# Optimization experiments

Measured on AMD Instinct MI355X. Metric: run time of the kernel, lower is better.

## Reference

```python
import jax, jax.numpy as jnp
import numpy as np

NQ, NT, D = 8192, 8192, 128
EC, EQ, ET = 262144, 262144, 262144


def seg_softmax(logits, seg, num):
    # numerically stable segment softmax over a 1-D logits vector
    m = jax.ops.segment_max(logits, seg, num_segments=num)
    e = jnp.exp(logits - m[seg])
    s = jax.ops.segment_sum(e, seg, num_segments=num)
    return e / s[seg]


def _linear_params(key, din, dout):
    k1, k2 = jax.random.split(key)
    scale = 1.0 / np.sqrt(din)
    W = jax.random.uniform(k1, (din, dout), minval=-scale, maxval=scale, dtype=jnp.float32)
    b = jax.random.uniform(k2, (dout,), minval=-scale, maxval=scale, dtype=jnp.float32)
    return W, b


def setup_inputs():
    key = jax.random.key(0)
    ks = jax.random.split(key, 20)
    inp = {
        'Xq': jax.random.normal(ks[0], (NQ, D), dtype=jnp.float32),
        'edge_index_q': jax.random.randint(ks[1], (2, EQ), 0, NQ),
        'Xt': jax.random.normal(ks[2], (NT, D), dtype=jnp.float32),
        'edge_index_t': jax.random.randint(ks[3], (2, ET), 0, NT),
        'norm_q': jax.random.uniform(ks[4], (NQ, 1), dtype=jnp.float32),
        'norm_t': jax.random.uniform(ks[5], (NT, 1), dtype=jnp.float32),
        'cross_src': jax.random.randint(ks[6], (EC,), 0, NQ),
        'cross_dst': jax.random.randint(ks[7], (EC,), 0, NT),
        'node_mask': jnp.ones((NQ,), dtype=bool),
        'only_run_inter': 0,
    }
    names_dims = [
        ('ac_q', D, D), ('ac_t', D, D), ('vc_q', D, D), ('vc_t', D, D),
        ('mq', 2 * D, D), ('mt', 3 * D, D),
        ('aq', 2 * D, 1), ('vq', 2 * D, D), ('at', 2 * D, 1), ('vt', 2 * D, D),
    ]
    for i, (nm, din, dout) in enumerate(names_dims):
        W, b = _linear_params(ks[8 + i], din, dout)
        inp['W_' + nm] = W
        inp['b_' + nm] = b
    return inp


def reference(Xq, edge_index_q, Xt, edge_index_t, norm_q, norm_t, cross_src, cross_dst,
              node_mask, only_run_inter,
              W_ac_q, b_ac_q, W_ac_t, b_ac_t, W_vc_q, b_vc_q, W_vc_t, b_vc_t,
              W_mq, b_mq, W_mt, b_mt,
              W_aq, b_aq, W_vq, b_vq, W_at, b_at, W_vt, b_vt):
    elu = jax.nn.elu
    nq, nt, d = Xq.shape[0], Xt.shape[0], Xq.shape[1]

    # cross-graph attention logits: per (u, v) pair, dot of transformed features
    Xq_ac = elu(Xq @ W_ac_q + b_ac_q)
    Xt_ac = elu(Xt @ W_ac_t + b_ac_t)
    att_logits = jnp.sum(Xq_ac[cross_src] * Xt_ac[cross_dst], axis=-1)  # [EC]

    # t2q: aggregate target values into query nodes (faithful to original: values gathered by u indices)
    Xt_vc = elu(Xt @ W_vc_t + b_vc_t)
    att_u = seg_softmax(att_logits, cross_src, nq)[:, None]
    Xt2q = jax.ops.segment_sum(att_u * Xt_vc[cross_src], cross_src, num_segments=nq)
    Xq_merged = jnp.concatenate([Xq, Xt2q], axis=1) @ W_mq + b_mq

    # q2t: aggregate query values into target nodes, plus global query summary Q
    Xq_vc = elu(Xq @ W_vc_q + b_vc_q)
    att_v = seg_softmax(att_logits, cross_dst, nt)[:, None]
    Xq2t = jax.ops.segment_sum(att_v * Xq_vc[cross_src], cross_dst, num_segments=nt)
    Q = jnp.broadcast_to(jnp.mean(Xq, axis=0, keepdims=True), (nt, d))
    Xt_merged = jnp.concatenate([Xt, Xq2t, Q], axis=1) @ W_mt + b_mt

    if only_run_inter:
        return Xq_merged, Xt_merged

    # intra-graph edge-wise gather -> MLP -> softmax-scatter message passing
    msg_t = jnp.concatenate([Xt_merged[edge_index_t[0]], Xt_merged[edge_index_t[1]]], axis=1)  # [ET, 2D]
    a_t = seg_softmax((msg_t @ W_at + b_at)[:, 0], edge_index_t[1], nt)[:, None]
    Xt_out = jax.ops.segment_sum(a_t * (msg_t @ W_vt + b_vt), edge_index_t[1], num_segments=nt)

    msg_q = jnp.concatenate([Xq_merged[edge_index_q[0]], Xq_merged[edge_index_q[1]]], axis=1)  # [EQ, 2D]
    a_q = seg_softmax((msg_q @ W_aq + b_aq)[:, 0], edge_index_q[1], nq)[:, None]
    Xq_out = jax.ops.segment_sum(a_q * (msg_q @ W_vq + b_vq), edge_index_q[1], num_segments=nq)

    return Xq_out, Xt_out
```

## Files before the change

kernel.cpp:

```cpp
#include <hip/hip_runtime.h>
#include <math.h>


#define NBIN 8192
#define NB   128
#define DEGCAP 256

typedef _Float16 h2f __attribute__((ext_vector_type(2)));

__device__ __forceinline__ float elu1(float x) { return x > 0.f ? x : __expf(x) - 1.f; }

__device__ __forceinline__ unsigned short f2bf(float x) {
    unsigned u = __float_as_uint(x);
    u += 0x7FFF + ((u >> 16) & 1);
    return (unsigned short)(u >> 16);
}
__device__ __forceinline__ float bflo(unsigned u) { return __uint_as_float(u << 16); }
__device__ __forceinline__ float bfhi(unsigned u) { return __uint_as_float(u & 0xFFFF0000u); }
__device__ __forceinline__ unsigned short f2h(float x) {
    return __builtin_bit_cast(unsigned short, (_Float16)x);
}

__device__ __forceinline__ float dot8_f16(const uint4 a, const uint4 b, float d) {
#if __has_builtin(__builtin_amdgcn_fdot2)
    d = __builtin_amdgcn_fdot2(__builtin_bit_cast(h2f, a.x), __builtin_bit_cast(h2f, b.x), d, false);
    d = __builtin_amdgcn_fdot2(__builtin_bit_cast(h2f, a.y), __builtin_bit_cast(h2f, b.y), d, false);
    d = __builtin_amdgcn_fdot2(__builtin_bit_cast(h2f, a.z), __builtin_bit_cast(h2f, b.z), d, false);
    d = __builtin_amdgcn_fdot2(__builtin_bit_cast(h2f, a.w), __builtin_bit_cast(h2f, b.w), d, false);
#else
    const unsigned ua[4] = { a.x, a.y, a.z, a.w };
    const unsigned ub[4] = { b.x, b.y, b.z, b.w };
    #pragma unroll
    for (int t = 0; t < 4; ++t) {
        const h2f ha = __builtin_bit_cast(h2f, ua[t]);
        const h2f hb = __builtin_bit_cast(h2f, ub[t]);
        d = fmaf((float)ha.x, (float)hb.x, d);
        d = fmaf((float)ha.y, (float)hb.y, d);
    }
#endif
    return d;
}

struct GemmJob {
    const float* A0; const float* A1; const int* rowmask1;
    const float* W00; const float* W01;
    const float* W10; const float* W11;
    const float* bias0; const float* bias1;
    float* C0; float* C1;
    unsigned short* Cb0; unsigned short* Cb1;
    unsigned short* Ch0; unsigned short* Ch1;
    const float* gvw; float* gvo;
    int act;
};

__global__ __launch_bounds__(256) void gemm_big(GemmJob j0, GemmJob j1)
{
    const GemmJob j = blockIdx.z ? j1 : j0;
    const int out = blockIdx.y >> 1;
    const int c0 = (blockIdx.y & 1) * 64;
    const int r0 = blockIdx.x * 128;
    __shared__ float As[32][132];
    __shared__ float Ws[32][64];
    const int tid = threadIdx.x;
    const int tr = tid >> 4, tc = tid & 15;
    float acc[8][4] = {};

    const float* A_pass[2] = { j.A0, j.A1 };
    const float* W_pass[2] = { out ? j.W01 : j.W00, out ? j.W11 : j.W10 };

    for (int p = 0; p < 2; ++p) {
        const float* A = A_pass[p];
        if (!A) break;
        const float* W = W_pass[p];
        const int* rm = (p == 1) ? j.rowmask1 : nullptr;
        for (int kc = 0; kc < 4; ++kc) {
            {
                const int k4 = (tid & 7) * 4;
                const int rb = tid >> 3;
                #pragma unroll
                for (int i = 0; i < 4; ++i) {
                    const int r = rb + 32 * i;
                    float4 v = *(const float4*)(A + (size_t)(r0 + r) * 128 + kc * 32 + k4);
                    if (rm && rm[r0 + r] == 0) v = make_float4(0.f, 0.f, 0.f, 0.f);
                    As[k4 + 0][r] = v.x; As[k4 + 1][r] = v.y;
                    As[k4 + 2][r] = v.z; As[k4 + 3][r] = v.w;
                }
                const int cc = (tid & 15) * 4;
                const int kb = tid >> 4;
                #pragma unroll
                for (int i = 0; i < 2; ++i) {
                    const int k = kb + 16 * i;
                    *(float4*)&Ws[k][cc] = *(const float4*)(W + (size_t)(kc * 32 + k) * 128 + c0 + cc);
                }
            }
            __syncthreads();
            #pragma unroll 4
            for (int k = 0; k < 32; ++k) {
                const float4 a0 = *(const float4*)&As[k][tr * 4];
                const float4 a1 = *(const float4*)&As[k][64 + tr * 4];
                const float4 w  = *(const float4*)&Ws[k][tc * 4];
                const float ar[8] = {a0.x, a0.y, a0.z, a0.w, a1.x, a1.y, a1.z, a1.w};
                #pragma unroll
                for (int i = 0; i < 8; ++i) {
                    acc[i][0] = fmaf(ar[i], w.x, acc[i][0]);
                    acc[i][1] = fmaf(ar[i], w.y, acc[i][1]);
                    acc[i][2] = fmaf(ar[i], w.z, acc[i][2]);
                    acc[i][3] = fmaf(ar[i], w.w, acc[i][3]);
                }
            }
            __syncthreads();
        }
    }

    float4 bv = make_float4(0.f, 0.f, 0.f, 0.f);
    const float* bias = out ? j.bias1 : j.bias0;
    if (bias) bv = *(const float4*)(bias + c0 + tc * 4);
    float* C = out ? j.C1 : j.C0;
    unsigned short* Cb = out ? j.Cb1 : j.Cb0;
    unsigned short* Ch = out ? j.Ch1 : j.Ch0;
    const int dogv = (j.gvw != nullptr) && (out == 0);
    float4 wv4 = make_float4(0.f, 0.f, 0.f, 0.f);
    if (dogv) wv4 = *(const float4*)(j.gvw + c0 + tc * 4);
    float pacc[8];
    #pragma unroll
    for (int i = 0; i < 8; ++i) {
        const int row = r0 + (i >> 2) * 64 + tr * 4 + (i & 3);
        float4 o;
        o.x = acc[i][0] + bv.x; o.y = acc[i][1] + bv.y;
        o.z = acc[i][2] + bv.z; o.w = acc[i][3] + bv.w;
        if (j.act) { o.x = elu1(o.x); o.y = elu1(o.y); o.z = elu1(o.z); o.w = elu1(o.w); }
        pacc[i] = o.x * wv4.x + o.y * wv4.y + o.z * wv4.z + o.w * wv4.w;
        if (C) {
            *(float4*)(C + (size_t)row * 128 + c0 + tc * 4) = o;
        } else if (Cb) {
            uint2 pk;
            pk.x = (unsigned)f2bf(o.x) | ((unsigned)f2bf(o.y) << 16);
            pk.y = (unsigned)f2bf(o.z) | ((unsigned)f2bf(o.w) << 16);
            *(uint2*)(Cb + (size_t)row * 128 + c0 + tc * 4) = pk;
        } else {
            uint2 pk;
            pk.x = (unsigned)f2h(o.x) | ((unsigned)f2h(o.y) << 16);
            pk.y = (unsigned)f2h(o.z) | ((unsigned)f2h(o.w) << 16);
            *(uint2*)(Ch + (size_t)row * 128 + c0 + tc * 4) = pk;
        }
    }
    if (dogv) {
        #pragma unroll
        for (int i = 0; i < 8; ++i) {
            float p = pacc[i];
            p += __shfl_xor(p, 1, 64); p += __shfl_xor(p, 2, 64);
            p += __shfl_xor(p, 4, 64); p += __shfl_xor(p, 8, 64);
            if (tc == 0)
                atomicAdd(j.gvo + r0 + (i >> 2) * 64 + tr * 4 + (i & 3), p);
        }
    }
}

__global__ __launch_bounds__(256) void hist_priv(
    const int* __restrict__ cs, const int* __restrict__ cd,
    const int* __restrict__ et1, const int* __restrict__ eq1,
    int* __restrict__ mask_src, unsigned short* __restrict__ partial,
    int EC, int ET, int EQ)
{
    __shared__ int h[NBIN];
    const int k = blockIdx.x, a = blockIdx.y, tid = threadIdx.x;
    const int* idxs[3] = { cd, et1, eq1 };
    const int Es[3] = { EC, ET, EQ };
    for (int b = tid; b < NBIN; b += 256) h[b] = 0;
    __syncthreads();
    const int E = Es[a];
    const int per = (E + NB - 1) / NB;
    const int lo = k * per;
    const int hi = min(E, lo + per);
    const int* idx = idxs[a];
    for (int e = lo + tid; e < hi; e += 256) {
        atomicAdd(&h[idx[e]], 1);
        if (a == 0) mask_src[cs[e]] = 1;
    }
    __syncthreads();
    unsigned short* P = partial + ((size_t)a * NB + k) * NBIN;
    for (int b = tid; b < NBIN; b += 256) P[b] = (unsigned short)h[b];
}

__global__ void binprefix_kernel(unsigned short* __restrict__ partial, int* __restrict__ cnt)
{
    const int bin = blockIdx.x * 256 + threadIdx.x;
    const int a = blockIdx.y;
    unsigned short* P = partial + (size_t)a * NB * NBIN;
    int s = 0;
    #pragma unroll 4
    for (int k = 0; k < NB; ++k) {
        const int p = P[(size_t)k * NBIN + bin];
        P[(size_t)k * NBIN + bin] = (unsigned short)s;
        s += p;
    }
    cnt[a * NBIN + bin] = s;
}

__global__ __launch_bounds__(1024) void scan3_kernel(const int* __restrict__ cnt, int* __restrict__ offs)
{
    const int b = blockIdx.x;
    const int* c = cnt + (size_t)b * NBIN;
    int* o = offs + (size_t)b * (NBIN + 1);
    __shared__ int sums[1024];
    const int tid = threadIdx.x;
    int loc[8]; int s = 0;
    #pragma unroll
    for (int j = 0; j < 8; ++j) { loc[j] = s; s += c[tid * 8 + j]; }
    sums[tid] = s;
    __syncthreads();
    for (int off = 1; off < 1024; off <<= 1) {
        int v = 0;
        if (tid >= off) v = sums[tid - off];
        __syncthreads();
        sums[tid] += v;
        __syncthreads();
    }
    const int ex = tid ? sums[tid - 1] : 0;
    #pragma unroll
    for (int j = 0; j < 8; ++j) o[tid * 8 + j] = ex + loc[j];
    if (tid == 1023) o[NBIN] = sums[1023];
}

__global__ __launch_bounds__(256) void scatter_det(
    const int* __restrict__ cs, const int* __restrict__ cd,
    const int* __restrict__ et0, const int* __restrict__ et1,
    const int* __restrict__ eq0, const int* __restrict__ eq1,
    const unsigned short* __restrict__ partial, const int* __restrict__ offs,
    int* __restrict__ ids_cd, int* __restrict__ ids_t, int* __restrict__ ids_q,
    int EC, int ET, int EQ)
{
    __shared__ int cur[NBIN];
    const int k = blockIdx.x, a = blockIdx.y, tid = threadIdx.x;
    const int Es[3] = { EC, ET, EQ };
    const int* seg[3] = { cd, et1, eq1 };
    const int* pay[3] = { cs, et0, eq0 };
    int* dst[3] = { ids_cd, ids_t, ids_q };
    const unsigned short* P = partial + ((size_t)a * NB + k) * NBIN;
    const int* off = offs + (size_t)a * (NBIN + 1);
    for (int b = tid; b < NBIN; b += 256) cur[b] = off[b] + (int)P[b];
    __syncthreads();
    const int E = Es[a];
    const int per = (E + NB - 1) / NB;
    const int lo = k * per;
    const int hi = min(E, lo + per);
    const int* sg = seg[a]; const int* pl = pay[a]; int* dd = dst[a];
    for (int e = lo + tid; e < hi; e += 256) {
        const int pos = atomicAdd(&cur[sg[e]], 1);
        dd[pos] = pl[e];
    }
}

__global__ void colsum_kernel(const float* __restrict__ X, float* __restrict__ sum)
{
    const int c = threadIdx.x & 127;
    const int half = threadIdx.x >> 7;
    float s = 0.f;
    #pragma unroll 8
    for (int j = 0; j < 64; ++j) {
        const int r = blockIdx.x * 128 + half + 2 * j;
        s += X[(size_t)r * 128 + c];
    }
    atomicAdd(&sum[c], s);
}

__global__ __launch_bounds__(512) void mt_extra_kernel(
    const float* __restrict__ Qsum, const float* __restrict__ Wmt,
    const float* __restrict__ bmt, float* __restrict__ outv, int M)
{
    __shared__ float red[4][128];
    const int c = threadIdx.x & 127, kq = threadIdx.x >> 7;
    const float inv = 1.0f / (float)M;
    float acc = 0.f;
    #pragma unroll 4
    for (int k = kq * 32; k < kq * 32 + 32; ++k)
        acc = fmaf(Qsum[k] * inv, Wmt[(size_t)(256 + k) * 128 + c], acc);
    red[kq][c] = acc;
    __syncthreads();
    if (kq == 0) outv[c] = bmt[c] + red[0][c] + red[1][c] + red[2][c] + red[3][c];
}

__device__ __forceinline__ void gather_chunk_bf(
    const unsigned int* __restrict__ rows, int myid, float wv, int rem,
    int half, int cl, float4& acc)
{
    const int npairs = (rem + 1) >> 1;
    int j = 0;
    for (; j + 4 <= npairs; j += 4) {
        const int e0 = 2 * j + half, e1 = e0 + 2, e2 = e0 + 4, e3 = e0 + 6;
        const int s0 = __shfl(myid, e0, 64); const float w0 = __shfl(wv, e0, 64);
        const int s1 = __shfl(myid, e1, 64); const float w1 = __shfl(wv, e1, 64);
        const int s2 = __shfl(myid, e2, 64); const float w2 = __shfl(wv, e2, 64);
        const int s3 = __shfl(myid, e3, 64); const float w3 = __shfl(wv, e3, 64);
        const uint2 v0 = *(const uint2*)(rows + (size_t)s0 * 64 + cl * 2);
        const uint2 v1 = *(const uint2*)(rows + (size_t)s1 * 64 + cl * 2);
        const uint2 v2 = *(const uint2*)(rows + (size_t)s2 * 64 + cl * 2);
        const uint2 v3 = *(const uint2*)(rows + (size_t)s3 * 64 + cl * 2);
        acc.x = fmaf(w0, bflo(v0.x), acc.x); acc.y = fmaf(w0, bfhi(v0.x), acc.y);
        acc.z = fmaf(w0, bflo(v0.y), acc.z); acc.w = fmaf(w0, bfhi(v0.y), acc.w);
        acc.x = fmaf(w1, bflo(v1.x), acc.x); acc.y = fmaf(w1, bfhi(v1.x), acc.y);
        acc.z = fmaf(w1, bflo(v1.y), acc.z); acc.w = fmaf(w1, bfhi(v1.y), acc.w);
        acc.x = fmaf(w2, bflo(v2.x), acc.x); acc.y = fmaf(w2, bfhi(v2.x), acc.y);
        acc.z = fmaf(w2, bflo(v2.y), acc.z); acc.w = fmaf(w2, bfhi(v2.y), acc.w);
        acc.x = fmaf(w3, bflo(v3.x), acc.x); acc.y = fmaf(w3, bfhi(v3.x), acc.y);
        acc.z = fmaf(w3, bflo(v3.y), acc.z); acc.w = fmaf(w3, bfhi(v3.y), acc.w);
    }
    for (; j < npairs; ++j) {
        const int e = 2 * j + half;
        const int sv = __shfl(myid, e, 64); const float we = __shfl(wv, e, 64);
        const uint2 v = *(const uint2*)(rows + (size_t)sv * 64 + cl * 2);
        acc.x = fmaf(we, bflo(v.x), acc.x); acc.y = fmaf(we, bfhi(v.x), acc.y);
        acc.z = fmaf(we, bflo(v.y), acc.z); acc.w = fmaf(we, bfhi(v.y), acc.w);
    }
}

__global__ __launch_bounds__(256) void seg_agg_intra(
    const int* ot, const int* it, const float* nlt, const unsigned int* rt,
    const float* xt, const float* ebt, float* outt,
    const int* oq, const int* iq, const float* nlq, const unsigned int* rq,
    const float* xq, const float* ebq, float* outq, int nseg)
{
    const int* offs; const int* ids; const float* nl; const unsigned int* rows;
    const float* extra; const float* eb; float* out;
    if (blockIdx.y == 0) { offs = ot; ids = it; nl = nlt; rows = rt; extra = xt; eb = ebt; out = outt; }
    else                 { offs = oq; ids = iq; nl = nlq; rows = rq; extra = xq; eb = ebq; out = outq; }
    const int wid = (int)((blockIdx.x * blockDim.x + threadIdx.x) >> 6);
    const int lane = threadIdx.x & 63;
    if (wid >= nseg) return;
    const int lo = offs[wid], hi = offs[wid + 1];
    const int deg = hi - lo;
    if (deg == 0) {
        *(float2*)(out + (size_t)wid * 128 + lane * 2) = make_float2(0.f, 0.f);
        return;
    }
    const int half = lane >> 5, cl = lane & 31;
    float s;
    float4 acc = make_float4(0.f, 0.f, 0.f, 0.f);
    if (deg <= 64) {
        int myid = 0; float l = -3.4e38f;
        if (lane < deg) { myid = ids[lo + lane]; l = nl[myid]; }
        float m = l;
        #pragma unroll
        for (int t = 32; t; t >>= 1) m = fmaxf(m, __shfl_xor(m, t, 64));
        const float wv = (lane < deg) ? __expf(l - m) : 0.f;
        s = wv;
        gather_chunk_bf(rows, myid, wv, deg, half, cl, acc);
    } else {
        float m = -3.4e38f;
        for (int i = lo + lane; i < hi; i += 64) m = fmaxf(m, nl[ids[i]]);
        #pragma unroll
        for (int t = 32; t; t >>= 1) m = fmaxf(m, __shfl_xor(m, t, 64));
        s = 0.f;
        for (int base = lo; base < hi; base += 64) {
            const int rem = min(64, hi - base);
            int myid = 0; float wv = 0.f;
            if (lane < rem) { myid = ids[base + lane]; wv = __expf(nl[myid] - m); }
            s += wv;
            gather_chunk_bf(rows, myid, wv, rem, half, cl, acc);
        }
    }
    #pragma unroll
    for (int t = 32; t; t >>= 1) s += __shfl_xor(s, t, 64);
    acc.x += __shfl_xor(acc.x, 32, 64); acc.y += __shfl_xor(acc.y, 32, 64);
    acc.z += __shfl_xor(acc.z, 32, 64); acc.w += __shfl_xor(acc.w, 32, 64);
    if (half == 0) {
        const float inv = 1.f / s;
        const float4 xv = *(const float4*)(extra + (size_t)wid * 128 + cl * 4);
        const float4 bv = *(const float4*)(eb + cl * 4);
        float4 o;
        o.x = fmaf(acc.x, inv, xv.x + bv.x);
        o.y = fmaf(acc.y, inv, xv.y + bv.y);
        o.z = fmaf(acc.z, inv, xv.z + bv.z);
        o.w = fmaf(acc.w, inv, xv.w + bv.w);
        *(float4*)(out + (size_t)wid * 128 + cl * 4) = o;
    }
}

__global__ __launch_bounds__(256) void seg_agg_cross(
    const int* __restrict__ offs, const int* __restrict__ ids,
    const unsigned int* __restrict__ Aqh, const unsigned int* __restrict__ Ath,
    const unsigned int* __restrict__ Vqb, float* __restrict__ out, int nseg)
{
    __shared__ unsigned int atrowh[4][64];
    __shared__ float lcache[4][DEGCAP];
    const int w = threadIdx.x >> 6;
    const int lane = threadIdx.x & 63;
    const int wid = blockIdx.x * 4 + w;
    if (wid >= nseg) return;
    const int lo = offs[wid], hi = offs[wid + 1];
    const int deg = hi - lo;
    if (deg == 0) {
        *(float2*)(out + (size_t)wid * 128 + lane * 2) = make_float2(0.f, 0.f);
        return;
    }
    atrowh[w][lane] = Ath[(size_t)wid * 64 + lane];
    __threadfence_block();

    const int half = lane >> 5, cl = lane & 31;
    float s;
    float4 acc = make_float4(0.f, 0.f, 0.f, 0.f);

    if (deg <= 64) {
        int myid = 0; float d = -3.4e38f;
        if (lane < deg) {
            myid = ids[lo + lane];
            const unsigned int* ar = Aqh + (size_t)myid * 64;
            d = 0.f;
            #pragma unroll
            for (int k = 0; k < 64; k += 4)
                d = dot8_f16(*(const uint4*)(ar + k), *(const uint4*)&atrowh[w][k], d);
        }
        float m = d;
        #pragma unroll
        for (int t = 32; t; t >>= 1) m = fmaxf(m, __shfl_xor(m, t, 64));
        const float wv = (lane < deg) ? __expf(d - m) : 0.f;
        s = wv;
        gather_chunk_bf(Vqb, myid, wv, deg, half, cl, acc);
    } else {
        float m = -3.4e38f;
        for (int base = lo; base < hi; base += 64) {
            const int i = base + lane;
            if (i < hi) {
                const int src = ids[i];
                const unsigned int* ar = Aqh + (size_t)src * 64;
                float d = 0.f;
                #pragma unroll
                for (int k = 0; k < 64; k += 4)
                    d = dot8_f16(*(const uint4*)(ar + k), *(const uint4*)&atrowh[w][k], d);
                const int li = i - lo;
                if (li < DEGCAP) lcache[w][li] = d;
                m = fmaxf(m, d);
            }
        }
        #pragma unroll
        for (int t = 32; t; t >>= 1) m = fmaxf(m, __shfl_xor(m, t, 64));
        __threadfence_block();
        s = 0.f;
        for (int base = lo; base < hi; base += 64) {
            const int rem = min(64, hi - base);
            int myid = 0; float wv = 0.f;
            if (lane < rem) {
                myid = ids[base + lane];
                const int li = base - lo + lane;
                float d;
                if (li < DEGCAP) d = lcache[w][li];
                else {
                    const unsigned int* ar = Aqh + (size_t)myid * 64;
                    d = 0.f;
                    for (int k = 0; k < 64; k += 4)
                        d = dot8_f16(*(const uint4*)(ar + k), *(const uint4*)&atrowh[w][k], d);
                }
                wv = __expf(d - m);
            }
            s += wv;
            gather_chunk_bf(Vqb, myid, wv, rem, half, cl, acc);
        }
    }
    #pragma unroll
    for (int t = 32; t; t >>= 1) s += __shfl_xor(s, t, 64);
    acc.x += __shfl_xor(acc.x, 32, 64); acc.y += __shfl_xor(acc.y, 32, 64);
    acc.z += __shfl_xor(acc.z, 32, 64); acc.w += __shfl_xor(acc.w, 32, 64);
    if (half == 0) {
        const float inv = 1.f / s;
        float4 o;
        o.x = acc.x * inv; o.y = acc.y * inv; o.z = acc.z * inv; o.w = acc.w * inv;
        *(float4*)(out + (size_t)wid * 128 + cl * 4) = o;
    }
}

extern "C" void kernel_launch(void* const* d_in, const int* in_sizes, int n_in,
                              void* d_out, int out_size, void* d_ws, size_t ws_size,
                              hipStream_t stream)
{
    const float* Xq    = (const float*)d_in[0];
    const int*   eqidx = (const int*)d_in[1];
    const float* Xt    = (const float*)d_in[2];
    const int*   etidx = (const int*)d_in[3];
    const int*   cs    = (const int*)d_in[6];
    const int*   cd    = (const int*)d_in[7];
    const float* W_ac_q = (const float*)d_in[10]; const float* b_ac_q = (const float*)d_in[11];
    const float* W_ac_t = (const float*)d_in[12]; const float* b_ac_t = (const float*)d_in[13];
    const float* W_vc_q = (const float*)d_in[14]; const float* b_vc_q = (const float*)d_in[15];
    const float* W_vc_t = (const float*)d_in[16]; const float* b_vc_t = (const float*)d_in[17];
    const float* W_mq   = (const float*)d_in[18]; const float* b_mq   = (const float*)d_in[19];
    const float* W_mt   = (const float*)d_in[20]; const float* b_mt   = (const float*)d_in[21];
    const float* W_aq   = (const float*)d_in[22];
    const float* W_vq   = (const float*)d_in[24]; const float* b_vq   = (const float*)d_in[25];
    const float* W_at   = (const float*)d_in[26];
    const float* W_vt   = (const float*)d_in[28]; const float* b_vt   = (const float*)d_in[29];

    const int NQ = in_sizes[0] / 128;
    const int EQ = in_sizes[1] / 2;
    const int NT = in_sizes[2] / 128;
    const int ET = in_sizes[3] / 2;
    const int EC = in_sizes[6];

    const int* eq0 = eqidx;  const int* eq1 = eqidx + EQ;
    const int* et0 = etidx;  const int* et1 = etidx + ET;

    float* base = (float*)d_ws;
    size_t off = 0;
    auto alloc = [&](size_t n) { float* p = base + off; off += n; return p; };
    float* N1 = alloc((size_t)NT * 128);
    float* N2 = alloc((size_t)NQ * 128);
    float* N3 = alloc((size_t)NT * 128);
    float* N4 = alloc((size_t)NT * 128);
    unsigned int* A0h = (unsigned int*)alloc((size_t)NQ * 64);
    unsigned int* A1h = (unsigned int*)alloc((size_t)NT * 64);
    unsigned short* B0 = (unsigned short*)alloc((size_t)NQ * 64);
    unsigned short* B1 = (unsigned short*)alloc((size_t)NT * 64);
    unsigned short* B2 = (unsigned short*)alloc((size_t)NQ * 64);
    float* mte  = alloc(128);
    float* st0v = alloc((size_t)NT);
    float* sq0v = alloc((size_t)NQ);
    int* mask_src = (int*)alloc((size_t)NQ);
    float* Qsum   = alloc(128);
    const size_t zero_bytes = ((size_t)NT + NQ + NQ + 128) * 4;
    int* cnt  = (int*)alloc((size_t)3 * NBIN);
    int* offs = (int*)alloc((size_t)3 * (NBIN + 1));
    unsigned short* partial = (unsigned short*)alloc((size_t)3 * NB * NBIN / 2);
    int* ids_cd = (int*)alloc((size_t)EC);
    int* ids_t  = (int*)alloc((size_t)ET);
    int* ids_q  = (int*)alloc((size_t)EQ);

    float* Xq_out = (float*)d_out;
    float* Xt_out = (float*)d_out + (size_t)NQ * 128;

    const int* offs_cd = offs;
    const int* offs_t  = offs + (NBIN + 1);
    const int* offs_q  = offs + 2 * (NBIN + 1);

    hipMemsetAsync(st0v, 0, zero_bytes, stream);

    hist_priv<<<dim3(NB, 3), 256, 0, stream>>>(cs, cd, et1, eq1, mask_src, partial, EC, ET, EQ);
    binprefix_kernel<<<dim3(NBIN / 256, 3), 256, 0, stream>>>(partial, cnt);
    scan3_kernel<<<3, 1024, 0, stream>>>(cnt, offs);
    scatter_det<<<dim3(NB, 3), 256, 0, stream>>>(cs, cd, et0, et1, eq0, eq1, partial, offs,
                                                 ids_cd, ids_t, ids_q, EC, ET, EQ);

    colsum_kernel<<<NQ / 128, 256, 0, stream>>>(Xq, Qsum);
    mt_extra_kernel<<<1, 512, 0, stream>>>(Qsum, W_mt, b_mt, mte, NQ);

    GemmJob jq{}, jt{};
    jq.A0 = Xq; jq.W00 = W_ac_q; jq.W01 = W_vc_q; jq.bias0 = b_ac_q; jq.bias1 = b_vc_q;
    jq.Ch0 = (unsigned short*)A0h; jq.Cb1 = B0; jq.act = 1;
    jt.A0 = Xt; jt.W00 = W_ac_t; jt.W01 = W_vc_t; jt.bias0 = b_ac_t; jt.bias1 = b_vc_t;
    jt.Ch0 = (unsigned short*)A1h; jt.C1 = N3; jt.act = 1;
    gemm_big<<<dim3(NQ / 128, 4, 2), 256, 0, stream>>>(jq, jt);

    seg_agg_cross<<<(NT + 3) / 4, 256, 0, stream>>>(offs_cd, ids_cd, A0h, A1h,
                                                    (const unsigned int*)B0, N4, NT);

    GemmJob mq{}, mt{};
    mq.A0 = Xq; mq.W00 = W_mq;               mq.A1 = N3; mq.W10 = W_mq + 128 * 128;
    mq.rowmask1 = mask_src; mq.bias0 = b_mq; mq.C0 = N2;
    mq.gvw = W_aq; mq.gvo = sq0v; mq.act = 0;
    mt.A0 = Xt; mt.W00 = W_mt;               mt.A1 = N4; mt.W10 = W_mt + 128 * 128;
    mt.bias0 = mte; mt.C0 = N1;
    mt.gvw = W_at; mt.gvo = st0v; mt.act = 0;
    gemm_big<<<dim3(NQ / 128, 2, 2), 256, 0, stream>>>(mq, mt);

    GemmJob ut{}, uq{};
    ut.A0 = N1; ut.W00 = W_vt; ut.W01 = W_vt + 128 * 128; ut.Cb0 = B1; ut.C1 = Xt_out; ut.act = 0;
    uq.A0 = N2; uq.W00 = W_vq; uq.W01 = W_vq + 128 * 128; uq.Cb0 = B2; uq.C1 = Xq_out; uq.act = 0;
    gemm_big<<<dim3(NT / 128, 4, 2), 256, 0, stream>>>(ut, uq);

    seg_agg_intra<<<dim3((NT + 3) / 4, 2), 256, 0, stream>>>(
        offs_t, ids_t, st0v, (const unsigned int*)B1, Xt_out, b_vt, Xt_out,
        offs_q, ids_q, sq0v, (const unsigned int*)B2, Xq_out, b_vq, Xq_out, NT);
}
```

Measured before the change: 269.2 us.

## Merge independent preprocessing kernels into horizontally fused launches; use online softmax in aggregation

Merges the first GEMM, the histogram and the column sum into one launch (stage1), and the scatter and mt_extra into another (stage3). Blocks pick their sub-task from blockIdx, which cuts launch count and lets independent work run side by side on the GPU. Segment aggregation kernels replace the two-pass and small/large degree branches with one online-softmax loop using a running max and rescaling. This drops the DEGCAP logit cache, and the fused kernels use a shared 32KB LDS buffer that may lower occupancy for the GEMM blocks.

```diff
diff --git a/kernel.cpp b/kernel.cpp
--- a/kernel.cpp
+++ b/kernel.cpp
@@ -4,7 +4,6 @@
 
 #define NBIN 8192
 #define NB   128
-#define DEGCAP 256
 
 typedef _Float16 h2f __attribute__((ext_vector_type(2)));
 
@@ -53,15 +52,15 @@
     int act;
 };
 
-__global__ __launch_bounds__(256) void gemm_big(GemmJob j0, GemmJob j1)
-{
-    const GemmJob j = blockIdx.z ? j1 : j0;
-    const int out = blockIdx.y >> 1;
-    const int c0 = (blockIdx.y & 1) * 64;
-    const int r0 = blockIdx.x * 128;
-    __shared__ float As[32][132];
-    __shared__ float Ws[32][64];
-    const int tid = threadIdx.x;
+#define GEMM_LDS_BYTES (32 * 132 * 4 + 32 * 64 * 4)
+
+__device__ void gemm_body(const GemmJob& j, int bx, int by, char* smem, int tid)
+{
+    const int out = by >> 1;
+    const int c0 = (by & 1) * 64;
+    const int r0 = bx * 128;
+    float (*As)[132] = (float(*)[132])smem;
+    float (*Ws)[64]  = (float(*)[64])(smem + 32 * 132 * 4);
     const int tr = tid >> 4, tc = tid & 15;
     float acc[8][4] = {};
 
@@ -156,14 +155,19 @@
     }
 }
 
-__global__ __launch_bounds__(256) void hist_priv(
-    const int* __restrict__ cs, const int* __restrict__ cd,
-    const int* __restrict__ et1, const int* __restrict__ eq1,
-    int* __restrict__ mask_src, unsigned short* __restrict__ partial,
-    int EC, int ET, int EQ)
-{
-    __shared__ int h[NBIN];
-    const int k = blockIdx.x, a = blockIdx.y, tid = threadIdx.x;
+__global__ __launch_bounds__(256) void gemm_big(GemmJob j0, GemmJob j1)
+{
+    __shared__ __align__(16) char smem[GEMM_LDS_BYTES];
+    gemm_body(blockIdx.z ? j1 : j0, blockIdx.x, blockIdx.y, smem, threadIdx.x);
+}
+
+__device__ void hist_body(int k, int a, int* h,
+                          const int* __restrict__ cs, const int* __restrict__ cd,
+                          const int* __restrict__ et1, const int* __restrict__ eq1,
+                          int* __restrict__ mask_src, unsigned short* __restrict__ partial,
+                          int EC, int ET, int EQ)
+{
+    const int tid = threadIdx.x;
     const int* idxs[3] = { cd, et1, eq1 };
     const int Es[3] = { EC, ET, EQ };
     for (int b = tid; b < NBIN; b += 256) h[b] = 0;
@@ -180,6 +184,39 @@
     __syncthreads();
     unsigned short* P = partial + ((size_t)a * NB + k) * NBIN;
     for (int b = tid; b < NBIN; b += 256) P[b] = (unsigned short)h[b];
+}
+
+__device__ void colsum_body(int bx, const float* __restrict__ X, float* __restrict__ sum)
+{
+    const int c = threadIdx.x & 127;
+    const int half = threadIdx.x >> 7;
+    float s = 0.f;
+    #pragma unroll 8
+    for (int j = 0; j < 64; ++j) {
+        const int r = bx * 128 + half + 2 * j;
+        s += X[(size_t)r * 128 + c];
+    }
+    atomicAdd(&sum[c], s);
+}
+
+__global__ __launch_bounds__(256) void stage1(
+    GemmJob j0, GemmJob j1, int ngx,
+    const int* cs, const int* cd, const int* et1, const int* eq1,
+    int* mask_src, unsigned short* partial, int EC, int ET, int EQ,
+    const float* Xq, float* Qsum)
+{
+    __shared__ __align__(16) char smem[32768];
+    int b = blockIdx.x;
+    const int NG = ngx * 8;
+    if (b < NG) {
+        const int x = b % ngx;
+        const int r = b / ngx;
+        gemm_body((r >> 2) ? j1 : j0, x, r & 3, smem, threadIdx.x);
+    } else if ((b -= NG) < 3 * NB) {
+        hist_body(b % NB, b / NB, (int*)smem, cs, cd, et1, eq1, mask_src, partial, EC, ET, EQ);
+    } else {
+        colsum_body(b - 3 * NB, Xq, Qsum);
+    }
 }
 
 __global__ void binprefix_kernel(unsigned short* __restrict__ partial, int* __restrict__ cnt)
@@ -222,7 +259,7 @@
     if (tid == 1023) o[NBIN] = sums[1023];
 }
 
-__global__ __launch_bounds__(256) void scatter_det(
+__device__ void scatter_body(int k, int a, int* cur,
     const int* __restrict__ cs, const int* __restrict__ cd,
     const int* __restrict__ et0, const int* __restrict__ et1,
     const int* __restrict__ eq0, const int* __restrict__ eq1,
@@ -230,8 +267,7 @@
     int* __restrict__ ids_cd, int* __restrict__ ids_t, int* __restrict__ ids_q,
     int EC, int ET, int EQ)
 {
-    __shared__ int cur[NBIN];
-    const int k = blockIdx.x, a = blockIdx.y, tid = threadIdx.x;
+    const int tid = threadIdx.x;
     const int Es[3] = { EC, ET, EQ };
     const int* seg[3] = { cd, et1, eq1 };
     const int* pay[3] = { cs, et0, eq0 };
@@ -251,33 +287,35 @@
     }
 }
 
-__global__ void colsum_kernel(const float* __restrict__ X, float* __restrict__ sum)
-{
-    const int c = threadIdx.x & 127;
-    const int half = threadIdx.x >> 7;
-    float s = 0.f;
-    #pragma unroll 8
-    for (int j = 0; j < 64; ++j) {
-        const int r = blockIdx.x * 128 + half + 2 * j;
-        s += X[(size_t)r * 128 + c];
-    }
-    atomicAdd(&sum[c], s);
-}
-
-__global__ __launch_bounds__(512) void mt_extra_kernel(
+__device__ void mt_extra_body(float* red,
     const float* __restrict__ Qsum, const float* __restrict__ Wmt,
     const float* __restrict__ bmt, float* __restrict__ outv, int M)
 {
-    __shared__ float red[4][128];
-    const int c = threadIdx.x & 127, kq = threadIdx.x >> 7;
+    const int c = threadIdx.x & 127, h = threadIdx.x >> 7;
     const float inv = 1.0f / (float)M;
     float acc = 0.f;
     #pragma unroll 4
-    for (int k = kq * 32; k < kq * 32 + 32; ++k)
+    for (int k = h * 64; k < h * 64 + 64; ++k)
         acc = fmaf(Qsum[k] * inv, Wmt[(size_t)(256 + k) * 128 + c], acc);
-    red[kq][c] = acc;
+    red[h * 128 + c] = acc;
     __syncthreads();
-    if (kq == 0) outv[c] = bmt[c] + red[0][c] + red[1][c] + red[2][c] + red[3][c];
+    if (h == 0) outv[c] = bmt[c] + red[c] + red[128 + c];
+}
+
+__global__ __launch_bounds__(256) void stage3(
+    const int* cs, const int* cd,
+    const int* et0, const int* et1, const int* eq0, const int* eq1,
+    const unsigned short* partial, const int* offs,
+    int* ids_cd, int* ids_t, int* ids_q, int EC, int ET, int EQ,
+    const float* Qsum, const float* Wmt, const float* bmt, float* mte, int M)
+{
+    __shared__ __align__(16) char smem[32768];
+    const int b = blockIdx.x;
+    if (b < 3 * NB)
+        scatter_body(b % NB, b / NB, (int*)smem, cs, cd, et0, et1, eq0, eq1,
+                     partial, offs, ids_cd, ids_t, ids_q, EC, ET, EQ);
+    else
+        mt_extra_body((float*)smem, Qsum, Wmt, bmt, mte, M);
 }
 
 __device__ __forceinline__ void gather_chunk_bf(
@@ -328,36 +366,27 @@
     const int lane = threadIdx.x & 63;
     if (wid >= nseg) return;
     const int lo = offs[wid], hi = offs[wid + 1];
-    const int deg = hi - lo;
-    if (deg == 0) {
+    if (lo == hi) {
         *(float2*)(out + (size_t)wid * 128 + lane * 2) = make_float2(0.f, 0.f);
         return;
     }
     const int half = lane >> 5, cl = lane & 31;
-    float s;
+    float m = -3.4e38f, s = 0.f;
     float4 acc = make_float4(0.f, 0.f, 0.f, 0.f);
-    if (deg <= 64) {
+    for (int base = lo; base < hi; base += 64) {
+        const int rem = min(64, hi - base);
         int myid = 0; float l = -3.4e38f;
-        if (lane < deg) { myid = ids[lo + lane]; l = nl[myid]; }
-        float m = l;
+        if (lane < rem) { myid = ids[base + lane]; l = nl[myid]; }
+        float mc = l;
         #pragma unroll
-        for (int t = 32; t; t >>= 1) m = fmaxf(m, __shfl_xor(m, t, 64));
-        const float wv = (lane < deg) ? __expf(l - m) : 0.f;
-        s = wv;
-        gather_chunk_bf(rows, myid, wv, deg, half, cl, acc);
-    } else {
-        float m = -3.4e38f;
-        for (int i = lo + lane; i < hi; i += 64) m = fmaxf(m, nl[ids[i]]);
-        #pragma unroll
-        for (int t = 32; t; t >>= 1) m = fmaxf(m, __shfl_xor(m, t, 64));
-        s = 0.f;
-        for (int base = lo; base < hi; base += 64) {
-            const int rem = min(64, hi - base);
-            int myid = 0; float wv = 0.f;
-            if (lane < rem) { myid = ids[base + lane]; wv = __expf(nl[myid] - m); }
-            s += wv;
-            gather_chunk_bf(rows, myid, wv, rem, half, cl, acc);
-        }
+        for (int t = 32; t; t >>= 1) mc = fmaxf(mc, __shfl_xor(mc, t, 64));
+        const float nm = fmaxf(m, mc);
+        const float alpha = __expf(m - nm);
+        const float wv = (lane < rem) ? __expf(l - nm) : 0.f;
+        s = s * alpha + wv;
+        acc.x *= alpha; acc.y *= alpha; acc.z *= alpha; acc.w *= alpha;
+        m = nm;
+        gather_chunk_bf(rows, myid, wv, rem, half, cl, acc);
     }
     #pragma unroll
     for (int t = 32; t; t >>= 1) s += __shfl_xor(s, t, 64);
@@ -382,14 +411,12 @@
     const unsigned int* __restrict__ Vqb, float* __restrict__ out, int nseg)
 {
     __shared__ unsigned int atrowh[4][64];
-    __shared__ float lcache[4][DEGCAP];
     const int w = threadIdx.x >> 6;
     const int lane = threadIdx.x & 63;
     const int wid = blockIdx.x * 4 + w;
     if (wid >= nseg) return;
     const int lo = offs[wid], hi = offs[wid + 1];
-    const int deg = hi - lo;
-    if (deg == 0) {
+    if (lo == hi) {
         *(float2*)(out + (size_t)wid * 128 + lane * 2) = make_float2(0.f, 0.f);
         return;
     }
@@ -397,64 +424,29 @@
     __threadfence_block();
 
     const int half = lane >> 5, cl = lane & 31;
-    float s;
+    float m = -3.4e38f, s = 0.f;
     float4 acc = make_float4(0.f, 0.f, 0.f, 0.f);
-
-    if (deg <= 64) {
+    for (int base = lo; base < hi; base += 64) {
+        const int rem = min(64, hi - base);
         int myid = 0; float d = -3.4e38f;
-        if (lane < deg) {
-            myid = ids[lo + lane];
+        if (lane < rem) {
+            myid = ids[base + lane];
             const unsigned int* ar = Aqh + (size_t)myid * 64;
             d = 0.f;
             #pragma unroll
             for (int k = 0; k < 64; k += 4)
                 d = dot8_f16(*(const uint4*)(ar + k), *(const uint4*)&atrowh[w][k], d);
         }
-        float m = d;
+        float mc = d;
         #pragma unroll
-        for (int t = 32; t; t >>= 1) m = fmaxf(m, __shfl_xor(m, t, 64));
-        const float wv = (lane < deg) ? __expf(d - m) : 0.f;
-        s = wv;
-        gather_chunk_bf(Vqb, myid, wv, deg, half, cl, acc);
-    } else {
-        float m = -3.4e38f;
-        for (int base = lo; base < hi; base += 64) {
-            const int i = base + lane;
-            if (i < hi) {
-                const int src = ids[i];
-                const unsigned int* ar = Aqh + (size_t)src * 64;
-                float d = 0.f;
-                #pragma unroll
-                for (int k = 0; k < 64; k += 4)
-                    d = dot8_f16(*(const uint4*)(ar + k), *(const uint4*)&atrowh[w][k], d);
-                const int li = i - lo;
-                if (li < DEGCAP) lcache[w][li] = d;
-                m = fmaxf(m, d);
-            }
-        }
-        #pragma unroll
-        for (int t = 32; t; t >>= 1) m = fmaxf(m, __shfl_xor(m, t, 64));
-        __threadfence_block();
-        s = 0.f;
-        for (int base = lo; base < hi; base += 64) {
-            const int rem = min(64, hi - base);
-            int myid = 0; float wv = 0.f;
-            if (lane < rem) {
-                myid = ids[base + lane];
-                const int li = base - lo + lane;
-                float d;
-                if (li < DEGCAP) d = lcache[w][li];
-                else {
-                    const unsigned int* ar = Aqh + (size_t)myid * 64;
-                    d = 0.f;
-                    for (int k = 0; k < 64; k += 4)
-                        d = dot8_f16(*(const uint4*)(ar + k), *(const uint4*)&atrowh[w][k], d);
-                }
-                wv = __expf(d - m);
-            }
-            s += wv;
-            gather_chunk_bf(Vqb, myid, wv, rem, half, cl, acc);
-        }
+        for (int t = 32; t; t >>= 1) mc = fmaxf(mc, __shfl_xor(mc, t, 64));
+        const float nm = fmaxf(m, mc);
+        const float alpha = __expf(m - nm);
+        const float wv = (lane < rem) ? __expf(d - nm) : 0.f;
+        s = s * alpha + wv;
+        acc.x *= alpha; acc.y *= alpha; acc.z *= alpha; acc.w *= alpha;
+        m = nm;
+        gather_chunk_bf(Vqb, myid, wv, rem, half, cl, acc);
     }
     #pragma unroll
     for (int t = 32; t; t >>= 1) s += __shfl_xor(s, t, 64);
@@ -532,21 +524,22 @@
 
     hipMemsetAsync(st0v, 0, zero_bytes, stream);
 
-    hist_priv<<<dim3(NB, 3), 256, 0, stream>>>(cs, cd, et1, eq1, mask_src, partial, EC, ET, EQ);
-    binprefix_kernel<<<dim3(NBIN / 256, 3), 256, 0, stream>>>(partial, cnt);
-    scan3_kernel<<<3, 1024, 0, stream>>>(cnt, offs);
-    scatter_det<<<dim3(NB, 3), 256, 0, stream>>>(cs, cd, et0, et1, eq0, eq1, partial, offs,
-                                                 ids_cd, ids_t, ids_q, EC, ET, EQ);
-
-    colsum_kernel<<<NQ / 128, 256, 0, stream>>>(Xq, Qsum);
-    mt_extra_kernel<<<1, 512, 0, stream>>>(Qsum, W_mt, b_mt, mte, NQ);
-
     GemmJob jq{}, jt{};
     jq.A0 = Xq; jq.W00 = W_ac_q; jq.W01 = W_vc_q; jq.bias0 = b_ac_q; jq.bias1 = b_vc_q;
     jq.Ch0 = (unsigned short*)A0h; jq.Cb1 = B0; jq.act = 1;
     jt.A0 = Xt; jt.W00 = W_ac_t; jt.W01 = W_vc_t; jt.bias0 = b_ac_t; jt.bias1 = b_vc_t;
     jt.Ch0 = (unsigned short*)A1h; jt.C1 = N3; jt.act = 1;
-    gemm_big<<<dim3(NQ / 128, 4, 2), 256, 0, stream>>>(jq, jt);
+    const int ngx = NQ / 128;
+    const int nblk1 = ngx * 8 + 3 * NB + NQ / 128;
+    stage1<<<nblk1, 256, 0, stream>>>(jq, jt, ngx, cs, cd, et1, eq1,
+                                      mask_src, partial, EC, ET, EQ, Xq, Qsum);
+
+    binprefix_kernel<<<dim3(NBIN / 256, 3), 256, 0, stream>>>(partial, cnt);
+    scan3_kernel<<<3, 1024, 0, stream>>>(cnt, offs);
+
+    stage3<<<3 * NB + 1, 256, 0, stream>>>(cs, cd, et0, et1, eq0, eq1, partial, offs,
+                                           ids_cd, ids_t, ids_q, EC, ET, EQ,
+                                           Qsum, W_mt, b_mt, mte, NQ);
 
     seg_agg_cross<<<(NT + 3) / 4, 256, 0, stream>>>(offs_cd, ids_cd, A0h, A1h,
                                                     (const unsigned int*)B0, N4, NT);
```

Measured after the change: 336.8 us. 1.25x slower.
